# Kernel optimization log

Hardware: AMD Instinct MI355X
Metric: run time of the kernel (lower is better)

Reference implementation:

```python
import jax, jax.numpy as jnp
import numpy as np

N_NODES = 100000
N_EDGES = 3200000
N_FEAT = 128
H = 16
N_CLASSES = 10


def gcn_conv(x, edge_index, W, b, num_nodes):
    """PyG GCNConv (eval): add self-loops, symmetric norm, linear, scatter-add, bias."""
    xw = x @ W  # [N, out]
    loops = jnp.arange(num_nodes, dtype=edge_index.dtype)
    src = jnp.concatenate([edge_index[0], loops])  # message sources (x_j)
    dst = jnp.concatenate([edge_index[1], loops])  # aggregation targets
    ones = jnp.ones(src.shape[0], dtype=xw.dtype)
    deg = jax.ops.segment_sum(ones, dst, num_segments=num_nodes)
    dinv = jnp.where(deg > 0, jax.lax.rsqrt(deg), 0.0)
    norm = dinv[src] * dinv[dst]  # [E+N]
    msg = xw[src] * norm[:, None]  # gather + scale
    out = jax.ops.segment_sum(msg, dst, num_segments=num_nodes)
    return out + b


def setup_inputs() -> dict:
    key = jax.random.key(0)
    ks = jax.random.split(key, 8)
    x = jax.random.normal(ks[0], (N_NODES, N_FEAT), dtype=jnp.float32)
    edge_index = jax.random.randint(ks[1], (2, N_EDGES), 0, N_NODES, dtype=jnp.int64)
    topo_edges = jax.random.randint(ks[2], (2, N_EDGES), 0, N_NODES, dtype=jnp.int64)
    s1 = 1.0 / np.sqrt(N_FEAT)
    s4 = 1.0 / np.sqrt(2 * H)
    W1 = jax.random.normal(ks[3], (N_FEAT, H), dtype=jnp.float32) * s1
    b1 = jnp.zeros((H,), dtype=jnp.float32)
    W2 = jax.random.normal(ks[4], (N_FEAT, H), dtype=jnp.float32) * s1
    b2 = jnp.zeros((H,), dtype=jnp.float32)
    W4 = jax.random.normal(ks[5], (2 * H, N_CLASSES), dtype=jnp.float32) * s4
    b4 = jnp.zeros((N_CLASSES,), dtype=jnp.float32)
    return {"x": x, "edge_index": edge_index, "topo_edges": topo_edges,
            "W1": W1, "b1": b1, "W2": W2, "b2": b2, "W4": W4, "b4": b4}


def reference(x, edge_index, topo_edges, W1, b1, W2, b2, W4, b4):
    n = x.shape[0]
    # branch 1: structural edges
    x1 = jax.nn.relu(gcn_conv(x, edge_index, W1, b1, n))
    # branch 2: topological edges
    x2 = jax.nn.relu(gcn_conv(x, topo_edges, W2, b2, n))
    # dropout is identity in eval mode
    h = jnp.concatenate([x1, x2], axis=1)  # [N, 2H]
    logits = gcn_conv(h, edge_index, W4, b4, n)  # [N, num_classes]
    return jax.nn.log_softmax(logits, axis=1)
```

## Files before the change

kernel.cpp:

```cpp
#include <hip/hip_runtime.h>
#include <hip/hip_fp16.h>

#define N_NODES 100000
#define N_EDGES 3200000
#define NB 1024
#define BW 98
#define TBS (NB + 1)
#define CHUNK 16384
#define STCAP 4608


__global__ __launch_bounds__(512) void k_part(const int* __restrict__ ei, const int* __restrict__ te,
                                              unsigned* __restrict__ tmp1, unsigned* __restrict__ tmp2,
                                              unsigned short* __restrict__ tbl1, unsigned short* __restrict__ tbl2,
                                              int E, int PB) {
    extern __shared__ unsigned smem[];
    unsigned* sorted = smem;
    int* rank = (int*)(smem + CHUNK);
    int* loff = rank + NB;
    int* ps   = loff + NB;

    int gb = blockIdx.x;
    bool g2 = gb >= PB;
    const int* ed        = g2 ? te : ei;
    unsigned* tmp        = g2 ? tmp2 : tmp1;
    unsigned short* tbl  = g2 ? tbl2 : tbl1;
    int blk = g2 ? gb - PB : gb;
    int t = threadIdx.x;

    for (int i = t; i < NB; i += 512) rank[i] = 0;
    __syncthreads();
    int base = blk * CHUNK, end = min(base + CHUNK, E);
    int csize = end - base;
    for (int e = base + t; e < end; e += 512) atomicAdd(&rank[ed[E + e] / BW], 1);
    __syncthreads();
    int i2 = t * 2;
    int c0 = rank[i2], c1 = rank[i2 + 1];
    int tot = c0 + c1;
    ps[t] = tot;
    __syncthreads();
    #pragma unroll
    for (int d = 1; d < 512; d <<= 1) {
        int a = (t >= d) ? ps[t - d] : 0;
        __syncthreads();
        ps[t] += a;
        __syncthreads();
    }
    int excl = ps[t] - tot;
    loff[i2]     = excl;
    loff[i2 + 1] = excl + c0;
    rank[i2] = 0; rank[i2 + 1] = 0;
    __syncthreads();
    for (int e = base + t; e < end; e += 512) {
        int d = ed[E + e], s = ed[e];
        int b = d / BW;
        int r = atomicAdd(&rank[b], 1);
        sorted[loff[b] + r] = ((unsigned)(d - b * BW) << 20) | (unsigned)s;
    }
    __syncthreads();
    size_t tb = (size_t)blk * TBS;
    for (int i = t; i < NB; i += 512) tbl[tb + i] = (unsigned short)loff[i];
    if (t == 0) tbl[tb + NB] = (unsigned short)csize;
    size_t ob = (size_t)blk * CHUNK;
    for (int i = t; i < csize; i += 512) tmp[ob + i] = sorted[i];
}

__global__ __launch_bounds__(1024) void k_bbase(const unsigned short* __restrict__ tbl1,
                                                const unsigned short* __restrict__ tbl2,
                                                int* __restrict__ bbase1, int* __restrict__ bbase2, int PB) {
    __shared__ int ps[NB];
    const unsigned short* tbl = blockIdx.x ? tbl2 : tbl1;
    int* bbase                = blockIdx.x ? bbase2 : bbase1;
    int b = threadIdx.x;
    int tot = 0;
    for (int c = 0; c < PB; ++c) {
        size_t tb = (size_t)c * TBS;
        tot += (int)tbl[tb + b + 1] - (int)tbl[tb + b];
    }
    ps[b] = tot;
    __syncthreads();
    #pragma unroll
    for (int d = 1; d < NB; d <<= 1) {
        int a = (b >= d) ? ps[b - d] : 0;
        __syncthreads();
        ps[b] += a;
        __syncthreads();
    }
    bbase[b] = ps[b] - tot;
}

__global__ __launch_bounds__(256) void k_csr(
    const unsigned* __restrict__ tmp1, const unsigned* __restrict__ tmp2,
    const unsigned short* __restrict__ tbl1, const unsigned short* __restrict__ tbl2,
    const int* __restrict__ bbase1, const int* __restrict__ bbase2,
    unsigned* __restrict__ csr1, unsigned* __restrict__ csr2,
    int2* __restrict__ pk1, int2* __restrict__ pk2,
    float* __restrict__ dinv1, float* __restrict__ dinv2, int PB, int n) {
    __shared__ unsigned stage[STCAP];
    __shared__ int ncnt[BW], noff[BW], nrank[BW];
    __shared__ int ps[256];
    int gb = blockIdx.x;
    bool g2 = gb >= NB;
    int b = g2 ? gb - NB : gb;
    const unsigned* tmp       = g2 ? tmp2 : tmp1;
    const unsigned short* tbl = g2 ? tbl2 : tbl1;
    unsigned* csr             = g2 ? csr2 : csr1;
    int2* pk                  = g2 ? pk2 : pk1;
    float* dinv               = g2 ? dinv2 : dinv1;
    int bb = (g2 ? bbase2 : bbase1)[b];
    int t = threadIdx.x;
    if (t < BW) { ncnt[t] = 0; nrank[t] = 0; }
    int start = 0, len = 0;
    if (t < PB) {
        size_t tb = (size_t)t * TBS;
        start = tbl[tb + b];
        len = (int)tbl[tb + b + 1] - start;
    }
    ps[t] = len;
    __syncthreads();
    #pragma unroll
    for (int d = 1; d < 256; d <<= 1) {
        int a = (t >= d) ? ps[t - d] : 0;
        __syncthreads();
        ps[t] += a;
        __syncthreads();
    }
    int ofs = ps[t] - len;
    int sz = min(ps[255], STCAP);
    for (int i = 0; i < len; ++i) {
        int p = ofs + i;
        if (p < STCAP) stage[p] = tmp[(size_t)t * CHUNK + start + i];
    }
    __syncthreads();
    for (int i = t; i < sz; i += 256) atomicAdd(&ncnt[stage[i] >> 20], 1);
    __syncthreads();
    if (t == 0) {
        int run = 0;
        for (int k = 0; k < BW; ++k) { noff[k] = run; run += ncnt[k]; }
    }
    __syncthreads();
    int nd = b * BW + t;
    if (t < BW && nd < n) {
        pk[nd] = make_int2(bb + noff[t], ncnt[t]);
        dinv[nd] = rsqrtf((float)ncnt[t] + 1.f);
    }
    for (int i = t; i < sz; i += 256) {
        unsigned v = stage[i];
        int ld = v >> 20;
        int r = atomicAdd(&nrank[ld], 1);
        csr[bb + noff[ld] + r] = v & 0xFFFFFu;
    }
}

__global__ __launch_bounds__(256) void k_gemm12(
    const float* __restrict__ x,
    const float* __restrict__ W1, const float* __restrict__ W2,
    const float* __restrict__ dinv1, const float* __restrict__ dinv2,
    __half* __restrict__ xwh1, __half* __restrict__ xwh2, int n) {
    __shared__ float Wl[128][32];
    __shared__ float xs[8][128];
    int t = threadIdx.x;
    for (int i = t; i < 128 * 16; i += 256) {
        int k = i / 16, o = i % 16;
        Wl[k][o]      = W1[i];
        Wl[k][o + 16] = W2[i];
    }
    int node0 = blockIdx.x * 8;
    for (int i = t; i < 8 * 128; i += 256) {
        int r = i >> 7, c = i & 127;
        int node = node0 + r;
        xs[r][c] = (node < n) ? x[node * 128 + c] : 0.f;
    }
    __syncthreads();
    int r = t >> 5, o = t & 31;
    int node = node0 + r;
    if (node < n) {
        float s = 0.f;
        #pragma unroll
        for (int k = 0; k < 128; ++k) s += xs[r][k] * Wl[k][o];
        if (o < 16) xwh1[(size_t)node * 16 + o]        = __float2half(s * dinv1[node]);
        else        xwh2[(size_t)node * 16 + (o - 16)] = __float2half(s * dinv2[node]);
    }
}

__global__ __launch_bounds__(256) void k_gather12(
    const __half* __restrict__ xwh1, const __half* __restrict__ xwh2,
    const unsigned* __restrict__ csr1, const unsigned* __restrict__ csr2,
    const int2* __restrict__ pk1, const int2* __restrict__ pk2,
    const float* __restrict__ dinv1, const float* __restrict__ dinv2,
    const float* __restrict__ b1, const float* __restrict__ b2,
    __half* __restrict__ h, int n) {
    int t = threadIdx.x;
    int node = blockIdx.x * 8 + (t >> 5);
    int c = t & 31;
    if (node >= n) return;
    bool g1 = (c < 16);
    int cl = g1 ? c : (c - 16);
    const __half* xw    = g1 ? xwh1 : xwh2;
    const unsigned* csr = g1 ? csr1 : csr2;
    int2 oc = g1 ? pk1[node] : pk2[node];
    int o = oc.x, m = oc.y;
    float di = g1 ? dinv1[node] : dinv2[node];
    float acc = __half2float(xw[(size_t)node * 16 + cl]);
    int k = 0;
    for (; k + 4 <= m; k += 4) {
        unsigned j0 = csr[o + k], j1 = csr[o + k + 1], j2 = csr[o + k + 2], j3 = csr[o + k + 3];
        acc += __half2float(xw[(size_t)j0 * 16 + cl]);
        acc += __half2float(xw[(size_t)j1 * 16 + cl]);
        acc += __half2float(xw[(size_t)j2 * 16 + cl]);
        acc += __half2float(xw[(size_t)j3 * 16 + cl]);
    }
    for (; k < m; ++k) acc += __half2float(xw[(size_t)csr[o + k] * 16 + cl]);
    acc *= di;
    float bv = g1 ? b1[cl] : b2[cl];
    float v = acc + bv;
    h[(size_t)node * 32 + c] = __float2half(v > 0.f ? v : 0.f);
}

__global__ void k_gemm3(const __half* __restrict__ h, const float* __restrict__ W4,
                        const float* __restrict__ dinv1, __half* __restrict__ zsh, int n) {
    int i = blockIdx.x * blockDim.x + threadIdx.x;
    if (i >= n) return;
    float hr[32];
    const __half2* hp = (const __half2*)(h + (size_t)i * 32);
    #pragma unroll
    for (int q = 0; q < 16; ++q) {
        float2 f = __half22float2(hp[q]);
        hr[2 * q] = f.x; hr[2 * q + 1] = f.y;
    }
    float di = dinv1[i];
    #pragma unroll
    for (int c = 0; c < 10; ++c) {
        float s = 0.f;
        #pragma unroll
        for (int k = 0; k < 32; ++k) s += hr[k] * W4[k * 10 + c];
        zsh[(size_t)i * 16 + c] = __float2half(s * di);
    }
}

__global__ __launch_bounds__(256) void k_gather3(
    const __half* __restrict__ zsh,
    const unsigned* __restrict__ csr1, const int2* __restrict__ pk1,
    const float* __restrict__ dinv1,
    const float* __restrict__ b4, float* __restrict__ out, int n) {
    int t = threadIdx.x;
    int node = blockIdx.x * 16 + (t >> 4);
    int c = t & 15;
    if (node >= n) return;
    bool act = (c < 10);
    int cc = act ? c : 0;
    float di = dinv1[node];
    float acc = __half2float(zsh[(size_t)node * 16 + cc]);
    int2 oc = pk1[node];
    int o = oc.x, m = oc.y;
    int k = 0;
    for (; k + 4 <= m; k += 4) {
        unsigned j0 = csr1[o + k], j1 = csr1[o + k + 1], j2 = csr1[o + k + 2], j3 = csr1[o + k + 3];
        acc += __half2float(zsh[(size_t)j0 * 16 + cc]);
        acc += __half2float(zsh[(size_t)j1 * 16 + cc]);
        acc += __half2float(zsh[(size_t)j2 * 16 + cc]);
        acc += __half2float(zsh[(size_t)j3 * 16 + cc]);
    }
    for (; k < m; ++k) acc += __half2float(zsh[(size_t)csr1[o + k] * 16 + cc]);
    float logit = acc * di + b4[cc];
    float mv = act ? logit : -1e30f;
    #pragma unroll
    for (int w = 8; w >= 1; w >>= 1) mv = fmaxf(mv, __shfl_xor(mv, w, 16));
    float ex = act ? expf(logit - mv) : 0.f;
    float ssum = ex;
    #pragma unroll
    for (int w = 8; w >= 1; w >>= 1) ssum += __shfl_xor(ssum, w, 16);
    if (act) out[(size_t)node * 10 + c] = logit - mv - logf(ssum);
}

extern "C" void kernel_launch(void* const* d_in, const int* in_sizes, int n_in,
                              void* d_out, int out_size, void* d_ws, size_t ws_size,
                              hipStream_t stream) {
    const float* x  = (const float*)d_in[0];
    const int*   ei = (const int*)d_in[1];
    const int*   te = (const int*)d_in[2];
    const float* W1 = (const float*)d_in[3];
    const float* b1 = (const float*)d_in[4];
    const float* W2 = (const float*)d_in[5];
    const float* b2 = (const float*)d_in[6];
    const float* W4 = (const float*)d_in[7];
    const float* b4 = (const float*)d_in[8];
    float* out = (float*)d_out;

    const int N = N_NODES, E = N_EDGES;
    const int PB = (E + CHUNK - 1) / CHUNK;

    char* w = (char*)d_ws;
    auto alloc = [&](size_t bytes) { void* p = (void*)w; w += (bytes + 255) & ~255ull; return p; };
    unsigned* tmp1 = (unsigned*)alloc((size_t)PB * CHUNK * 4);
    unsigned* tmp2 = (unsigned*)alloc((size_t)PB * CHUNK * 4);
    unsigned* csr1 = (unsigned*)alloc((size_t)E * 4);
    unsigned* csr2 = (unsigned*)alloc((size_t)E * 4);
    unsigned short* tbl1 = (unsigned short*)alloc((size_t)PB * TBS * 2);
    unsigned short* tbl2 = (unsigned short*)alloc((size_t)PB * TBS * 2);
    int*   bbase1 = (int*)alloc((size_t)NB * 4);
    int*   bbase2 = (int*)alloc((size_t)NB * 4);
    int2*  pk1    = (int2*)alloc((size_t)N * 8);
    int2*  pk2    = (int2*)alloc((size_t)N * 8);
    float* dinv1  = (float*)alloc((size_t)N * 4);
    float* dinv2  = (float*)alloc((size_t)N * 4);
    __half* xwh1 = (__half*)tmp1;
    __half* xwh2 = xwh1 + (size_t)N * 16;
    __half* h    = xwh2 + (size_t)N * 16;
    __half* zsh  = h + (size_t)N * 32;

    const size_t PART_LDS = ((size_t)CHUNK + 2 * NB + 512) * 4;
    k_part<<<2 * PB, 512, PART_LDS, stream>>>(ei, te, tmp1, tmp2, tbl1, tbl2, E, PB);
    k_bbase<<<2, 1024, 0, stream>>>(tbl1, tbl2, bbase1, bbase2, PB);
    k_csr<<<2 * NB, 256, 0, stream>>>(tmp1, tmp2, tbl1, tbl2, bbase1, bbase2,
                                      csr1, csr2, pk1, pk2, dinv1, dinv2, PB, N);
    k_gemm12<<<(N + 7) / 8, 256, 0, stream>>>(x, W1, W2, dinv1, dinv2, xwh1, xwh2, N);
    k_gather12<<<(N + 7) / 8, 256, 0, stream>>>(xwh1, xwh2, csr1, csr2, pk1, pk2,
                                                dinv1, dinv2, b1, b2, h, N);
    k_gemm3<<<(N + 255) / 256, 256, 0, stream>>>(h, W4, dinv1, zsh, N);
    k_gather3<<<(N + 15) / 16, 256, 0, stream>>>(zsh, csr1, pk1, dinv1, b4, out, N);
}
```

Measured before the change: 443.6 us.

## Halve bucket count, transpose offset table, and cooperatively stage CSR bucket reads

Halves the number of destination buckets, each now 196 nodes wide, and stores the per-chunk bucket offset table transposed (bucket-major) so that the bbase and csr kernels read it contiguously. In k_csr the staging copy is done one wavefront per chunk run with 64 lanes reading consecutive elements, replacing the old loop where each thread serially copied its own run. The serial per-node offset scan on thread 0 becomes a parallel block scan. Larger buckets need a bigger dynamic LDS stage buffer and give fewer blocks, which may lower occupancy, and the capacity cap of 6912 could in principle truncate an unusually large bucket.

```diff
diff --git a/kernel.cpp b/kernel.cpp
--- a/kernel.cpp
+++ b/kernel.cpp
@@ -3,16 +3,16 @@
 
 #define N_NODES 100000
 #define N_EDGES 3200000
-#define NB 1024
-#define BW 98
-#define TBS (NB + 1)
+#define NB 512
+#define BW 196
 #define CHUNK 16384
-#define STCAP 4608
+#define PBMAX 256
+#define STCAP 6912
 
 
 __global__ __launch_bounds__(512) void k_part(const int* __restrict__ ei, const int* __restrict__ te,
                                               unsigned* __restrict__ tmp1, unsigned* __restrict__ tmp2,
-                                              unsigned short* __restrict__ tbl1, unsigned short* __restrict__ tbl2,
+                                              unsigned short* __restrict__ tblT1, unsigned short* __restrict__ tblT2,
                                               int E, int PB) {
     extern __shared__ unsigned smem[];
     unsigned* sorted = smem;
@@ -24,20 +24,18 @@
     bool g2 = gb >= PB;
     const int* ed        = g2 ? te : ei;
     unsigned* tmp        = g2 ? tmp2 : tmp1;
-    unsigned short* tbl  = g2 ? tbl2 : tbl1;
+    unsigned short* tbl  = g2 ? tblT2 : tblT1;
     int blk = g2 ? gb - PB : gb;
     int t = threadIdx.x;
 
-    for (int i = t; i < NB; i += 512) rank[i] = 0;
+    rank[t] = 0;
     __syncthreads();
     int base = blk * CHUNK, end = min(base + CHUNK, E);
     int csize = end - base;
     for (int e = base + t; e < end; e += 512) atomicAdd(&rank[ed[E + e] / BW], 1);
     __syncthreads();
-    int i2 = t * 2;
-    int c0 = rank[i2], c1 = rank[i2 + 1];
-    int tot = c0 + c1;
-    ps[t] = tot;
+    int v = rank[t];
+    ps[t] = v;
     __syncthreads();
     #pragma unroll
     for (int d = 1; d < 512; d <<= 1) {
@@ -46,10 +44,8 @@
         ps[t] += a;
         __syncthreads();
     }
-    int excl = ps[t] - tot;
-    loff[i2]     = excl;
-    loff[i2 + 1] = excl + c0;
-    rank[i2] = 0; rank[i2 + 1] = 0;
+    loff[t] = ps[t] - v;
+    rank[t] = 0;
     __syncthreads();
     for (int e = base + t; e < end; e += 512) {
         int d = ed[E + e], s = ed[e];
@@ -58,25 +54,22 @@
         sorted[loff[b] + r] = ((unsigned)(d - b * BW) << 20) | (unsigned)s;
     }
     __syncthreads();
-    size_t tb = (size_t)blk * TBS;
-    for (int i = t; i < NB; i += 512) tbl[tb + i] = (unsigned short)loff[i];
-    if (t == 0) tbl[tb + NB] = (unsigned short)csize;
+    tbl[(size_t)t * PB + blk] = (unsigned short)loff[t];
+    if (t == 0) tbl[(size_t)NB * PB + blk] = (unsigned short)csize;
     size_t ob = (size_t)blk * CHUNK;
     for (int i = t; i < csize; i += 512) tmp[ob + i] = sorted[i];
 }
 
-__global__ __launch_bounds__(1024) void k_bbase(const unsigned short* __restrict__ tbl1,
-                                                const unsigned short* __restrict__ tbl2,
-                                                int* __restrict__ bbase1, int* __restrict__ bbase2, int PB) {
+__global__ __launch_bounds__(512) void k_bbase(const unsigned short* __restrict__ tblT1,
+                                               const unsigned short* __restrict__ tblT2,
+                                               int* __restrict__ bbase1, int* __restrict__ bbase2, int PB) {
     __shared__ int ps[NB];
-    const unsigned short* tbl = blockIdx.x ? tbl2 : tbl1;
+    const unsigned short* tbl = blockIdx.x ? tblT2 : tblT1;
     int* bbase                = blockIdx.x ? bbase2 : bbase1;
     int b = threadIdx.x;
     int tot = 0;
-    for (int c = 0; c < PB; ++c) {
-        size_t tb = (size_t)c * TBS;
-        tot += (int)tbl[tb + b + 1] - (int)tbl[tb + b];
-    }
+    for (int c = 0; c < PB; ++c)
+        tot += (int)tbl[(size_t)(b + 1) * PB + c] - (int)tbl[(size_t)b * PB + c];
     ps[b] = tot;
     __syncthreads();
     #pragma unroll
@@ -91,32 +84,35 @@
 
 __global__ __launch_bounds__(256) void k_csr(
     const unsigned* __restrict__ tmp1, const unsigned* __restrict__ tmp2,
-    const unsigned short* __restrict__ tbl1, const unsigned short* __restrict__ tbl2,
+    const unsigned short* __restrict__ tblT1, const unsigned short* __restrict__ tblT2,
     const int* __restrict__ bbase1, const int* __restrict__ bbase2,
     unsigned* __restrict__ csr1, unsigned* __restrict__ csr2,
     int2* __restrict__ pk1, int2* __restrict__ pk2,
     float* __restrict__ dinv1, float* __restrict__ dinv2, int PB, int n) {
-    __shared__ unsigned stage[STCAP];
+    extern __shared__ unsigned stage[];
     __shared__ int ncnt[BW], noff[BW], nrank[BW];
+    __shared__ int rstart[PBMAX], rofs[PBMAX], rlen[PBMAX];
     __shared__ int ps[256];
     int gb = blockIdx.x;
     bool g2 = gb >= NB;
     int b = g2 ? gb - NB : gb;
     const unsigned* tmp       = g2 ? tmp2 : tmp1;
-    const unsigned short* tbl = g2 ? tbl2 : tbl1;
+    const unsigned short* tbl = g2 ? tblT2 : tblT1;
     unsigned* csr             = g2 ? csr2 : csr1;
     int2* pk                  = g2 ? pk2 : pk1;
     float* dinv               = g2 ? dinv2 : dinv1;
     int bb = (g2 ? bbase2 : bbase1)[b];
     int t = threadIdx.x;
-    if (t < BW) { ncnt[t] = 0; nrank[t] = 0; }
-    int start = 0, len = 0;
+    for (int u = t; u < BW; u += 256) { ncnt[u] = 0; nrank[u] = 0; }
+    int myLen = 0;
     if (t < PB) {
-        size_t tb = (size_t)t * TBS;
-        start = tbl[tb + b];
-        len = (int)tbl[tb + b + 1] - start;
-    }
-    ps[t] = len;
+        int s0 = tbl[(size_t)b * PB + t];
+        int s1 = tbl[(size_t)(b + 1) * PB + t];
+        rstart[t] = s0;
+        myLen = s1 - s0;
+        rlen[t] = myLen;
+    }
+    ps[t] = myLen;
     __syncthreads();
     #pragma unroll
     for (int d = 1; d < 256; d <<= 1) {
@@ -125,19 +121,31 @@
         ps[t] += a;
         __syncthreads();
     }
-    int ofs = ps[t] - len;
+    if (t < PB) rofs[t] = ps[t] - myLen;
     int sz = min(ps[255], STCAP);
-    for (int i = 0; i < len; ++i) {
-        int p = ofs + i;
-        if (p < STCAP) stage[p] = tmp[(size_t)t * CHUNK + start + i];
+    __syncthreads();
+    int wv = t >> 6, ln = t & 63;
+    for (int c = wv; c < PB; c += 4) {
+        int st = rstart[c], of = rofs[c], le = rlen[c];
+        for (int i = ln; i < le; i += 64) {
+            int p = of + i;
+            if (p < STCAP) stage[p] = tmp[(size_t)c * CHUNK + st + i];
+        }
     }
     __syncthreads();
     for (int i = t; i < sz; i += 256) atomicAdd(&ncnt[stage[i] >> 20], 1);
     __syncthreads();
-    if (t == 0) {
-        int run = 0;
-        for (int k = 0; k < BW; ++k) { noff[k] = run; run += ncnt[k]; }
-    }
+    int cv = (t < BW) ? ncnt[t] : 0;
+    ps[t] = cv;
+    __syncthreads();
+    #pragma unroll
+    for (int d = 1; d < 256; d <<= 1) {
+        int a = (t >= d) ? ps[t - d] : 0;
+        __syncthreads();
+        ps[t] += a;
+        __syncthreads();
+    }
+    if (t < BW) noff[t] = ps[t] - cv;
     __syncthreads();
     int nd = b * BW + t;
     if (t < BW && nd < n) {
@@ -296,8 +304,8 @@
     unsigned* tmp2 = (unsigned*)alloc((size_t)PB * CHUNK * 4);
     unsigned* csr1 = (unsigned*)alloc((size_t)E * 4);
     unsigned* csr2 = (unsigned*)alloc((size_t)E * 4);
-    unsigned short* tbl1 = (unsigned short*)alloc((size_t)PB * TBS * 2);
-    unsigned short* tbl2 = (unsigned short*)alloc((size_t)PB * TBS * 2);
+    unsigned short* tblT1 = (unsigned short*)alloc((size_t)(NB + 1) * PB * 2);
+    unsigned short* tblT2 = (unsigned short*)alloc((size_t)(NB + 1) * PB * 2);
     int*   bbase1 = (int*)alloc((size_t)NB * 4);
     int*   bbase2 = (int*)alloc((size_t)NB * 4);
     int2*  pk1    = (int2*)alloc((size_t)N * 8);
@@ -310,10 +318,11 @@
     __half* zsh  = h + (size_t)N * 32;
 
     const size_t PART_LDS = ((size_t)CHUNK + 2 * NB + 512) * 4;
-    k_part<<<2 * PB, 512, PART_LDS, stream>>>(ei, te, tmp1, tmp2, tbl1, tbl2, E, PB);
-    k_bbase<<<2, 1024, 0, stream>>>(tbl1, tbl2, bbase1, bbase2, PB);
-    k_csr<<<2 * NB, 256, 0, stream>>>(tmp1, tmp2, tbl1, tbl2, bbase1, bbase2,
-                                      csr1, csr2, pk1, pk2, dinv1, dinv2, PB, N);
+    const size_t CSR_LDS  = (size_t)STCAP * 4;
+    k_part<<<2 * PB, 512, PART_LDS, stream>>>(ei, te, tmp1, tmp2, tblT1, tblT2, E, PB);
+    k_bbase<<<2, NB, 0, stream>>>(tblT1, tblT2, bbase1, bbase2, PB);
+    k_csr<<<2 * NB, 256, CSR_LDS, stream>>>(tmp1, tmp2, tblT1, tblT2, bbase1, bbase2,
+                                            csr1, csr2, pk1, pk2, dinv1, dinv2, PB, N);
     k_gemm12<<<(N + 7) / 8, 256, 0, stream>>>(x, W1, W2, dinv1, dinv2, xwh1, xwh2, N);
     k_gather12<<<(N + 7) / 8, 256, 0, stream>>>(xwh1, xwh2, csr1, csr2, pk1, pk2,
                                                 dinv1, dinv2, b1, b2, h, N);
```

Measured after the change: 422.9 us. 4.7% less time.
